# Optimization experiments

Measured on AMD Instinct MI355X. Metric: run time of the kernel, lower is better.

The kernel has to match this reference:

```python
import math
import jax, jax.numpy as jnp
import numpy as np

B, S, H, DQ, DV = 2, 2048, 16, 192, 128
NEG_INF = jnp.float32(-1e30)


def setup_inputs() -> dict:
    key = jax.random.key(0)
    kq, kk, kv = jax.random.split(key, 3)
    q = jax.random.normal(kq, (B, S, H, DQ), dtype=jnp.float32)
    k = jax.random.normal(kk, (B, S, H, DQ), dtype=jnp.float32)
    v = jax.random.normal(kv, (B, S, H, DV), dtype=jnp.float32)
    return {"q": q, "k": k, "v": v}


def reference(q, k, v):
    # Causal MLA attention, BSHD layout, asymmetric QK vs V head dims.
    dq = q.shape[-1]
    scale = jnp.asarray(math.sqrt(1.0 / dq), dtype=q.dtype)  # default 1/sqrt(dq)
    # scores: [B, H, S, S]
    scores = jnp.einsum("bqhd,bkhd->bhqk", q, k) * scale
    s = q.shape[1]
    causal = jnp.tril(jnp.ones((s, s), dtype=bool))  # qidx >= kidx
    scores = jnp.where(causal[None, None, :, :], scores, NEG_INF)
    p = jax.nn.softmax(scores, axis=-1)
    # out: [B, S, H, DV]
    out = jnp.einsum("bhqk,bkhd->bqhd", p, v)
    return out
```

## Files before the change

### kernel.cpp

```cpp
#include <hip/hip_runtime.h>

#define B_ 2
#define S_ 2048
#define H_ 16
#define DQ_ 192
#define DV_ 128
#define SCL2 0.10411163731422901f

typedef short short8 __attribute__((ext_vector_type(8)));
typedef float f32x4 __attribute__((ext_vector_type(4)));
typedef float f32x16 __attribute__((ext_vector_type(16)));
typedef unsigned uint2v __attribute__((ext_vector_type(2)));

#define KG_BYTES ((size_t)25165824)
#define VG_BYTES ((size_t)16777216)

__device__ __forceinline__ unsigned short f2bf(float f) {
  union { float f; unsigned u; } x; x.f = f;
  unsigned r = x.u + 0x7FFFu + ((x.u >> 16) & 1u);
  return (unsigned short)(r >> 16);
}

__device__ __forceinline__ float hw_exp2(float x) {
  float r; asm("v_exp_f32 %0, %1" : "=v"(r) : "v"(x)); return r;
}
__device__ __forceinline__ unsigned cvtpk(float lo, float hi) {
  unsigned r; asm("v_cvt_pk_bf16_f32 %0, %1, %2" : "=v"(r) : "v"(lo), "v"(hi)); return r;
}
__device__ __forceinline__ float pl32max(float x) {
  uint2v r = __builtin_amdgcn_permlane32_swap(__float_as_uint(x), __float_as_uint(x), false, false);
  return fmaxf(__uint_as_float(r[0]), __uint_as_float(r[1]));
}
__device__ __forceinline__ float pl32add(float x) {
  uint2v r = __builtin_amdgcn_permlane32_swap(__float_as_uint(x), __float_as_uint(x), false, false);
  return __uint_as_float(r[0]) + __uint_as_float(r[1]);
}

#define GLL16(src, dst) \
  __builtin_amdgcn_global_load_lds((const __attribute__((address_space(1))) void*)(src), \
                                   (__attribute__((address_space(3))) void*)(dst), 16, 0, 0)

__global__ __launch_bounds__(256) void prep_k(const float* __restrict__ K,
                                              unsigned short* __restrict__ Kg) {
  int idx = blockIdx.x * 256 + threadIdx.x;
  int d4 = idx % 48; int r = idx / 48;
  int h = r % H_; r /= H_;
  int s = r % S_; int b = r / S_;
  float4 f = *(const float4*)(K + (size_t)((b * S_ + s) * H_ + h) * DQ_ + d4 * 4);
  ushort4 u; u.x = f2bf(f.x); u.y = f2bf(f.y); u.z = f2bf(f.z); u.w = f2bf(f.w);
  size_t rowb = (size_t)((b * H_ + h) * S_ + s) * (DQ_ * 2);
  int cb = (d4 * 8) ^ ((s & 7) << 4);
  *(ushort4*)((char*)Kg + rowb + cb) = u;
}

__global__ __launch_bounds__(256) void prep_v(const float* __restrict__ V,
                                              unsigned short* __restrict__ Vg) {
  __shared__ float lv[64][132];
  int blk = blockIdx.x;
  int tile = blk & 31, bh = blk >> 5;
  int b = bh >> 4, h = bh & 15;
  int tid = threadIdx.x;
  #pragma unroll
  for (int it = 0; it < 8; ++it) {
    int idx = it * 256 + tid;
    int s_in = idx >> 5, d4 = idx & 31;
    float4 f = *(const float4*)(V + (size_t)((b * S_ + tile * 64 + s_in) * H_ + h) * DV_ + d4 * 4);
    lv[s_in][d4 * 4 + 0] = f.x; lv[s_in][d4 * 4 + 1] = f.y;
    lv[s_in][d4 * 4 + 2] = f.z; lv[s_in][d4 * 4 + 3] = f.w;
  }
  __syncthreads();
  char* base = (char*)Vg + (size_t)blk * 16384;
  #pragma unroll
  for (int it = 0; it < 4; ++it) {
    int ch = it * 256 + tid;
    int pr = ch >> 4, ci = ch & 15;
    int orig = ci ^ (pr & 15);
    int dv = pr * 2 + (orig >> 3);
    int k0 = (orig & 7) * 8;
    short8 u;
    #pragma unroll
    for (int e = 0; e < 8; ++e) u[e] = (short)f2bf(lv[k0 + e][dv]);
    *(short8*)(base + ch * 16) = u;
  }
}

__launch_bounds__(256, 2)
__global__ void mla_fwd(const float* __restrict__ Q,
                        const unsigned short* __restrict__ Kg,
                        const unsigned short* __restrict__ Vg,
                        float* __restrict__ O) {
  __shared__ __align__(16) unsigned char SB[2][40960];

  const int tid  = threadIdx.x;
  const int wid  = tid >> 6;
  const int lane = tid & 63;
  const int l31  = lane & 31;
  const int hi   = lane >> 5;
  const int hi16 = hi * 16;

  const int i  = blockIdx.x;
  const int x  = i & 7;
  const int li = i >> 3;
  const int r_ = li >> 5;
  const int c  = li & 31;
  const int bh = x * 4 + (c >> 3);
  const int jj = c & 7;
  const int qtile = r_ ? jj : (15 - jj);
  const int b  = bh >> 4, h = bh & 15;

  const char* kg_bh = (const char*)Kg + (size_t)bh * S_ * (DQ_ * 2);
  const char* vg_bh = (const char*)Vg + (size_t)bh * 32 * 16384;

  const int wq0 = qtile * 128 + wid * 32;
  const int qln = wq0 + l31;

  short8 qf[12];
  {
    const size_t qoff = (size_t)((b * S_ + qln) * H_ + h) * DQ_;
    #pragma unroll
    for (int d0 = 0; d0 < 12; ++d0) {
      const float* p = Q + qoff + d0 * 16 + hi * 8;
      float4 f0 = *(const float4*)(p);
      float4 f1 = *(const float4*)(p + 4);
      short8 a;
      a[0] = f2bf(f0.x * SCL2); a[1] = f2bf(f0.y * SCL2);
      a[2] = f2bf(f0.z * SCL2); a[3] = f2bf(f0.w * SCL2);
      a[4] = f2bf(f1.x * SCL2); a[5] = f2bf(f1.y * SCL2);
      a[6] = f2bf(f1.z * SCL2); a[7] = f2bf(f1.w * SCL2);
      qf[d0] = a;
    }
  }

  f32x16 o[4];
  #pragma unroll
  for (int t2 = 0; t2 < 4; ++t2) o[t2] = (f32x16)0.0f;
  float m = -1e30f, l = 0.0f;

  const int kxor = (lane & 7) << 4;
  const int prl  = l31 >> 1;
  const int nb_  = (lane & 1) * 8 + hi;
  int voff[2][2];
  #pragma unroll
  for (int kh = 0; kh < 2; ++kh)
    #pragma unroll
    for (int ks = 0; ks < 2; ++ks) {
      int n = nb_ + kh * 4 + ks * 2;
      voff[kh][ks] = prl * 256 + ((n ^ prl) << 4);
    }

  const int ntiles = 2 * qtile + 2;

  const char* kS = kg_bh + wid * 10240 + lane * 16;
  const char* vS = vg_bh - 24576 + wid * 10240 + lane * 16;

  #define STAGE(buf)                                                       \
    do {                                                                   \
      _Pragma("unroll")                                                    \
      for (int ci = 0; ci < 10; ++ci) {                                    \
        const int cc = wid * 10 + ci;                                      \
        const char* src = (cc < 24) ? (kS + ci * 1024) : (vS + ci * 1024); \
        GLL16(src, &SB[buf][cc * 1024]);                                   \
      }                                                                    \
    } while (0)

  #define HALF(S, KH)                                                             \
    {                                                                             \
      const int khb = kbase + (KH) * 32;                                          \
      if (khb <= wq0 + 31) {                                                      \
        float p_[16];                                                             \
        _Pragma("unroll") for (int r = 0; r < 16; ++r) p_[r] = S[r];              \
        if (khb + 31 > wq0) {                                                     \
          const int rem = qln - khb - 4 * hi;                                     \
          _Pragma("unroll") for (int r = 0; r < 16; ++r) {                        \
            const int kof = (r & 3) + 8 * (r >> 2);                               \
            if (kof > rem) p_[r] = -1e30f;                                        \
          }                                                                       \
        }                                                                         \
        float mx = p_[0];                                                         \
        _Pragma("unroll") for (int r = 1; r < 16; ++r) mx = fmaxf(mx, p_[r]);     \
        mx = pl32max(mx);                                                         \
        if (__any(mx > m + 8.0f)) {                                               \
          float mn = fmaxf(m, mx);                                                \
          float al = hw_exp2(m - mn);                                             \
          _Pragma("unroll") for (int t2 = 0; t2 < 4; ++t2) o[t2] *= al;           \
          l *= al; m = mn;                                                        \
        }                                                                         \
        _Pragma("unroll") for (int r = 0; r < 16; ++r) p_[r] = hw_exp2(p_[r] - m);\
        float sum_ = 0.0f;                                                        \
        _Pragma("unroll") for (int r = 0; r < 16; ++r) sum_ += p_[r];             \
        l += sum_;                                                                \
        unsigned a_ = cvtpk(p_[0], p_[1]),   b2_ = cvtpk(p_[2], p_[3]);           \
        unsigned c_ = cvtpk(p_[4], p_[5]),   d_  = cvtpk(p_[6], p_[7]);           \
        unsigned e_ = cvtpk(p_[8], p_[9]),   f_  = cvtpk(p_[10], p_[11]);         \
        unsigned g_ = cvtpk(p_[12], p_[13]), h_  = cvtpk(p_[14], p_[15]);         \
        uint2v s02 = __builtin_amdgcn_permlane32_swap(a_, c_, false, false);      \
        uint2v s13 = __builtin_amdgcn_permlane32_swap(b2_, d_, false, false);     \
        uint2v s46 = __builtin_amdgcn_permlane32_swap(e_, g_, false, false);      \
        uint2v s57 = __builtin_amdgcn_permlane32_swap(f_, h_, false, false);      \
        union { unsigned u[4]; short8 s; } pb0, pb1;                              \
        pb0.u[0] = s02[0]; pb0.u[1] = s13[0]; pb0.u[2] = s02[1]; pb0.u[3] = s13[1];\
        pb1.u[0] = s46[0]; pb1.u[1] = s57[0]; pb1.u[2] = s46[1]; pb1.u[3] = s57[1];\
        __builtin_amdgcn_s_setprio(1);                                            \
        _Pragma("unroll") for (int t2 = 0; t2 < 4; ++t2) {                        \
          short8 va0 = *(const short8*)(vbb + t2 * 4096 + voff[KH][0]);           \
          o[t2] = __builtin_amdgcn_mfma_f32_32x32x16_bf16(va0, pb0.s, o[t2], 0, 0, 0); \
          short8 va1 = *(const short8*)(vbb + t2 * 4096 + voff[KH][1]);           \
          o[t2] = __builtin_amdgcn_mfma_f32_32x32x16_bf16(va1, pb1.s, o[t2], 0, 0, 0); \
        }                                                                         \
        __builtin_amdgcn_s_setprio(0);                                            \
      }                                                                           \
    }

  STAGE(0); kS += 24576; vS += 16384;
  __syncthreads();

  int cur = 0;
  for (int kt = 0; kt < ntiles; ++kt) {
    const int kbase = kt * 64;
    if (kt + 1 < ntiles) { STAGE(cur ^ 1); kS += 24576; vS += 16384; }

    const unsigned char* kb  = SB[cur];
    const unsigned char* vbb = SB[cur] + 24576;
    const bool active = (kbase <= wq0 + 31);

    if (active) {
      const char* kr0 = (const char*)kb + l31 * 384;
      const char* kr1 = kr0 + 32 * 384;
      f32x16 s0 = (f32x16)0.0f, s1 = (f32x16)0.0f;
      __builtin_amdgcn_s_setprio(1);
      #pragma unroll
      for (int d0 = 0; d0 < 12; ++d0) {
        const int col = (d0 * 32 + hi16) ^ kxor;
        s0 = __builtin_amdgcn_mfma_f32_32x32x16_bf16(*(const short8*)(kr0 + col), qf[d0], s0, 0, 0, 0);
        s1 = __builtin_amdgcn_mfma_f32_32x32x16_bf16(*(const short8*)(kr1 + col), qf[d0], s1, 0, 0, 0);
      }
      __builtin_amdgcn_s_setprio(0);

      HALF(s0, 0)
      HALF(s1, 1)
    }

    __syncthreads();
    cur ^= 1;
  }

  {
    float ll = pl32add(l);
    const float inv = 1.0f / ll;
    float* ob = O + (size_t)((b * S_ + qln) * H_ + h) * DV_;
    #pragma unroll
    for (int t2 = 0; t2 < 4; ++t2) {
      #pragma unroll
      for (int rr = 0; rr < 4; ++rr) {
        float4 st = { o[t2][rr * 4 + 0] * inv, o[t2][rr * 4 + 1] * inv,
                      o[t2][rr * 4 + 2] * inv, o[t2][rr * 4 + 3] * inv };
        *(float4*)(ob + t2 * 32 + rr * 8 + hi * 4) = st;
      }
    }
  }
  #undef STAGE
  #undef HALF
}

__launch_bounds__(256)
__global__ void mla_fwd_fb(const float* __restrict__ Q,
                           const float* __restrict__ K,
                           const float* __restrict__ V,
                           float* __restrict__ O) {
  __shared__ __align__(16) unsigned short Kl[2][32][200];
  __shared__ __align__(16) unsigned short Vt[2][128][40];
  __shared__ __align__(16) unsigned short Pl[4][16][40];
  const int tid = threadIdx.x, wid = tid >> 6, lane = tid & 63;
  const int l15 = lane & 15, g = lane >> 4;
  const int qtile = (int)gridDim.x - 1 - (int)blockIdx.x;
  const int bh = blockIdx.y, b = bh >> 4, h = bh & 15;
  const int q0w = qtile * 64 + wid * 16;
  const int krs = H_ * DQ_, vrs = H_ * DV_;
  short8 aq[6];
  {
    const int qoff = ((b * S_ + (q0w + l15)) * H_ + h) * DQ_;
    #pragma unroll
    for (int d0 = 0; d0 < 6; ++d0) {
      const float* p = Q + qoff + d0 * 32 + g * 8;
      float4 f0 = *(const float4*)(p); float4 f1 = *(const float4*)(p + 4);
      short8 a;
      a[0]=f2bf(f0.x); a[1]=f2bf(f0.y); a[2]=f2bf(f0.z); a[3]=f2bf(f0.w);
      a[4]=f2bf(f1.x); a[5]=f2bf(f1.y); a[6]=f2bf(f1.z); a[7]=f2bf(f1.w);
      aq[d0] = a;
    }
  }
  f32x4 o[8];
  #pragma unroll
  for (int t = 0; t < 8; ++t) o[t] = (f32x4)0.0f;
  float m[4], l[4];
  #pragma unroll
  for (int r = 0; r < 4; ++r) { m[r] = -1e30f; l[r] = 0.0f; }
  const int ntiles = qtile * 2 + 2;
  float4 kr[6], vr[4];
  {
    const float* Kb = K + ((b * S_) * H_ + h) * DQ_;
    #pragma unroll
    for (int i = 0; i < 6; ++i) { int idx = i*256+tid; int row = idx/48, c4 = idx%48;
      kr[i] = *(const float4*)(Kb + row*krs + c4*4); }
    const float* Vb = V + ((b * S_) * H_ + h) * DV_;
    #pragma unroll
    for (int i = 0; i < 4; ++i) { int idx = i*256+tid; int row = idx&31, c4 = idx>>5;
      vr[i] = *(const float4*)(Vb + row*vrs + c4*4); }
    #pragma unroll
    for (int i = 0; i < 6; ++i) { int idx = i*256+tid; int row = idx/48, c4 = idx%48;
      ushort4 u; u.x=f2bf(kr[i].x); u.y=f2bf(kr[i].y); u.z=f2bf(kr[i].z); u.w=f2bf(kr[i].w);
      *(ushort4*)&Kl[0][row][c4*4] = u; }
    #pragma unroll
    for (int i = 0; i < 4; ++i) { int idx = i*256+tid; int row = idx&31, c4 = idx>>5;
      Vt[0][c4*4+0][row]=f2bf(vr[i].x); Vt[0][c4*4+1][row]=f2bf(vr[i].y);
      Vt[0][c4*4+2][row]=f2bf(vr[i].z); Vt[0][c4*4+3][row]=f2bf(vr[i].w); }
  }
  __syncthreads();
  int cur = 0;
  for (int kt = 0; kt < ntiles; ++kt) {
    const int kbase = kt * 32;
    const bool pf = (kt + 1 < ntiles);
    if (pf) {
      const int nb = kbase + 32;
      const float* Kb = K + ((b*S_+nb)*H_ + h)*DQ_;
      #pragma unroll
      for (int i = 0; i < 6; ++i) { int idx = i*256+tid; int row = idx/48, c4 = idx%48;
        kr[i] = *(const float4*)(Kb + row*krs + c4*4); }
      const float* Vb = V + ((b*S_+nb)*H_ + h)*DV_;
      #pragma unroll
      for (int i = 0; i < 4; ++i) { int idx = i*256+tid; int row = idx&31, c4 = idx>>5;
        vr[i] = *(const float4*)(Vb + row*vrs + c4*4); }
    }
    f32x4 sa0 = (f32x4)0.0f, sa1 = (f32x4)0.0f;
    #pragma unroll
    for (int d0 = 0; d0 < 6; ++d0) {
      short8 b0 = *(const short8*)&Kl[cur][l15][d0*32 + g*8];
      sa0 = __builtin_amdgcn_mfma_f32_16x16x32_bf16(aq[d0], b0, sa0, 0, 0, 0);
      short8 b1 = *(const short8*)&Kl[cur][16+l15][d0*32 + g*8];
      sa1 = __builtin_amdgcn_mfma_f32_16x16x32_bf16(aq[d0], b1, sa1, 0, 0, 0);
    }
    float p0[4], p1[4];
    #pragma unroll
    for (int r = 0; r < 4; ++r) {
      const int qg = q0w + 4*g + r;
      float s0 = sa0[r]*SCL2, s1 = sa1[r]*SCL2;
      if (kbase + l15 > qg) s0 = -1e30f;
      if (kbase + 16 + l15 > qg) s1 = -1e30f;
      p0[r] = s0; p1[r] = s1;
    }
    #pragma unroll
    for (int r = 0; r < 4; ++r) {
      float rm = fmaxf(p0[r], p1[r]);
      #pragma unroll
      for (int off = 1; off < 16; off <<= 1) rm = fmaxf(rm, __shfl_xor(rm, off));
      float mn = fmaxf(m[r], rm);
      float alpha = exp2f(m[r] - mn); m[r] = mn;
      float e0 = exp2f(p0[r] - mn), e1 = exp2f(p1[r] - mn);
      p0[r] = e0; p1[r] = e1;
      float rsum = e0 + e1;
      #pragma unroll
      for (int off = 1; off < 16; off <<= 1) rsum += __shfl_xor(rsum, off);
      l[r] = l[r]*alpha + rsum;
      #pragma unroll
      for (int t = 0; t < 8; ++t) o[t][r] *= alpha;
    }
    #pragma unroll
    for (int r = 0; r < 4; ++r) {
      Pl[wid][4*g+r][l15]      = f2bf(p0[r]);
      Pl[wid][4*g+r][16+l15]   = f2bf(p1[r]);
    }
    short8 pa = *(const short8*)&Pl[wid][l15][g*8];
    #pragma unroll
    for (int t = 0; t < 8; ++t) {
      short8 vb = *(const short8*)&Vt[cur][t*16+l15][g*8];
      o[t] = __builtin_amdgcn_mfma_f32_16x16x32_bf16(pa, vb, o[t], 0, 0, 0);
    }
    if (pf) {
      #pragma unroll
      for (int i = 0; i < 6; ++i) { int idx = i*256+tid; int row = idx/48, c4 = idx%48;
        ushort4 u; u.x=f2bf(kr[i].x); u.y=f2bf(kr[i].y); u.z=f2bf(kr[i].z); u.w=f2bf(kr[i].w);
        *(ushort4*)&Kl[cur^1][row][c4*4] = u; }
      #pragma unroll
      for (int i = 0; i < 4; ++i) { int idx = i*256+tid; int row = idx&31, c4 = idx>>5;
        Vt[cur^1][c4*4+0][row]=f2bf(vr[i].x); Vt[cur^1][c4*4+1][row]=f2bf(vr[i].y);
        Vt[cur^1][c4*4+2][row]=f2bf(vr[i].z); Vt[cur^1][c4*4+3][row]=f2bf(vr[i].w); }
    }
    __syncthreads();
    cur ^= 1;
  }
  #pragma unroll
  for (int r = 0; r < 4; ++r) {
    const int qg = q0w + 4*g + r;
    const float inv = 1.0f / l[r];
    #pragma unroll
    for (int t = 0; t < 8; ++t)
      O[((b*S_+qg)*H_ + h)*DV_ + t*16 + l15] = o[t][r] * inv;
  }
}

extern "C" void kernel_launch(void* const* d_in, const int* in_sizes, int n_in,
                              void* d_out, int out_size, void* d_ws, size_t ws_size,
                              hipStream_t stream) {
  const float* q = (const float*)d_in[0];
  const float* k = (const float*)d_in[1];
  const float* v = (const float*)d_in[2];
  float* out = (float*)d_out;

  if (ws_size >= KG_BYTES + VG_BYTES) {
    unsigned short* Kg = (unsigned short*)d_ws;
    unsigned short* Vg = (unsigned short*)((char*)d_ws + KG_BYTES);
    prep_k<<<dim3((B_ * S_ * H_ * 48) / 256), dim3(256), 0, stream>>>(k, Kg);
    prep_v<<<dim3(B_ * H_ * 32), dim3(256), 0, stream>>>(v, Vg);
    mla_fwd<<<dim3(512), dim3(256), 0, stream>>>(q, Kg, Vg, out);
  } else {
    dim3 grid(S_ / 64, B_ * H_);
    mla_fwd_fb<<<grid, dim3(256), 0, stream>>>(q, k, v, out);
  }
}
```

Measured before the change: 94.97 us.

## Read V fragments directly from global memory and merge softmax over 64-key tile

Stops staging V tiles into shared memory. Each wave now loads its V MFMA operands straight from the pre-swizzled global bf16 buffer, which cuts the LDS footprint from 40KB to 24KB per buffer. The two 32-key softmax halves are merged into one 64-key pass with a tree max and tree sum, so there is one rescale check per tile. The block-to-tile mapping is also changed so causal q-tiles are interleaved across heads differently. In exchange, V reads now depend on global/L2 latency inside the inner loop instead of being prefetched into LDS.

```diff
diff --git a/kernel.cpp b/kernel.cpp
--- a/kernel.cpp
+++ b/kernel.cpp
@@ -89,7 +89,7 @@
                         const unsigned short* __restrict__ Kg,
                         const unsigned short* __restrict__ Vg,
                         float* __restrict__ O) {
-  __shared__ __align__(16) unsigned char SB[2][40960];
+  __shared__ __align__(16) unsigned char SB[2][24576];
 
   const int tid  = threadIdx.x;
   const int wid  = tid >> 6;
@@ -103,15 +103,15 @@
   const int li = i >> 3;
   const int r_ = li >> 5;
   const int c  = li & 31;
-  const int bh = x * 4 + (c >> 3);
-  const int jj = c & 7;
-  const int qtile = r_ ? jj : (15 - jj);
+  const int qt = c & 15;
+  const int pid = c >> 4;
+  const int bh = x * 4 + pid * 2 + r_;
   const int b  = bh >> 4, h = bh & 15;
 
   const char* kg_bh = (const char*)Kg + (size_t)bh * S_ * (DQ_ * 2);
   const char* vg_bh = (const char*)Vg + (size_t)bh * 32 * 16384;
 
-  const int wq0 = qtile * 128 + wid * 32;
+  const int wq0 = qt * 128 + wid * 32;
   const int qln = wq0 + l31;
 
   short8 qf[12];
@@ -148,83 +148,31 @@
       voff[kh][ks] = prl * 256 + ((n ^ prl) << 4);
     }
 
-  const int ntiles = 2 * qtile + 2;
-
-  const char* kS = kg_bh + wid * 10240 + lane * 16;
-  const char* vS = vg_bh - 24576 + wid * 10240 + lane * 16;
-
-  #define STAGE(buf)                                                       \
-    do {                                                                   \
-      _Pragma("unroll")                                                    \
-      for (int ci = 0; ci < 10; ++ci) {                                    \
-        const int cc = wid * 10 + ci;                                      \
-        const char* src = (cc < 24) ? (kS + ci * 1024) : (vS + ci * 1024); \
-        GLL16(src, &SB[buf][cc * 1024]);                                   \
-      }                                                                    \
+  const int ntiles = 2 * qt + 2;
+
+  const char* kS = kg_bh + wid * 6144 + lane * 16;
+  const int sdo = wid * 6144;
+
+  #define STAGE(buf)                                        \
+    do {                                                    \
+      _Pragma("unroll")                                     \
+      for (int ci = 0; ci < 6; ++ci)                        \
+        GLL16(kS + ci * 1024, &SB[buf][sdo + ci * 1024]);   \
     } while (0)
 
-  #define HALF(S, KH)                                                             \
-    {                                                                             \
-      const int khb = kbase + (KH) * 32;                                          \
-      if (khb <= wq0 + 31) {                                                      \
-        float p_[16];                                                             \
-        _Pragma("unroll") for (int r = 0; r < 16; ++r) p_[r] = S[r];              \
-        if (khb + 31 > wq0) {                                                     \
-          const int rem = qln - khb - 4 * hi;                                     \
-          _Pragma("unroll") for (int r = 0; r < 16; ++r) {                        \
-            const int kof = (r & 3) + 8 * (r >> 2);                               \
-            if (kof > rem) p_[r] = -1e30f;                                        \
-          }                                                                       \
-        }                                                                         \
-        float mx = p_[0];                                                         \
-        _Pragma("unroll") for (int r = 1; r < 16; ++r) mx = fmaxf(mx, p_[r]);     \
-        mx = pl32max(mx);                                                         \
-        if (__any(mx > m + 8.0f)) {                                               \
-          float mn = fmaxf(m, mx);                                                \
-          float al = hw_exp2(m - mn);                                             \
-          _Pragma("unroll") for (int t2 = 0; t2 < 4; ++t2) o[t2] *= al;           \
-          l *= al; m = mn;                                                        \
-        }                                                                         \
-        _Pragma("unroll") for (int r = 0; r < 16; ++r) p_[r] = hw_exp2(p_[r] - m);\
-        float sum_ = 0.0f;                                                        \
-        _Pragma("unroll") for (int r = 0; r < 16; ++r) sum_ += p_[r];             \
-        l += sum_;                                                                \
-        unsigned a_ = cvtpk(p_[0], p_[1]),   b2_ = cvtpk(p_[2], p_[3]);           \
-        unsigned c_ = cvtpk(p_[4], p_[5]),   d_  = cvtpk(p_[6], p_[7]);           \
-        unsigned e_ = cvtpk(p_[8], p_[9]),   f_  = cvtpk(p_[10], p_[11]);         \
-        unsigned g_ = cvtpk(p_[12], p_[13]), h_  = cvtpk(p_[14], p_[15]);         \
-        uint2v s02 = __builtin_amdgcn_permlane32_swap(a_, c_, false, false);      \
-        uint2v s13 = __builtin_amdgcn_permlane32_swap(b2_, d_, false, false);     \
-        uint2v s46 = __builtin_amdgcn_permlane32_swap(e_, g_, false, false);      \
-        uint2v s57 = __builtin_amdgcn_permlane32_swap(f_, h_, false, false);      \
-        union { unsigned u[4]; short8 s; } pb0, pb1;                              \
-        pb0.u[0] = s02[0]; pb0.u[1] = s13[0]; pb0.u[2] = s02[1]; pb0.u[3] = s13[1];\
-        pb1.u[0] = s46[0]; pb1.u[1] = s57[0]; pb1.u[2] = s46[1]; pb1.u[3] = s57[1];\
-        __builtin_amdgcn_s_setprio(1);                                            \
-        _Pragma("unroll") for (int t2 = 0; t2 < 4; ++t2) {                        \
-          short8 va0 = *(const short8*)(vbb + t2 * 4096 + voff[KH][0]);           \
-          o[t2] = __builtin_amdgcn_mfma_f32_32x32x16_bf16(va0, pb0.s, o[t2], 0, 0, 0); \
-          short8 va1 = *(const short8*)(vbb + t2 * 4096 + voff[KH][1]);           \
-          o[t2] = __builtin_amdgcn_mfma_f32_32x32x16_bf16(va1, pb1.s, o[t2], 0, 0, 0); \
-        }                                                                         \
-        __builtin_amdgcn_s_setprio(0);                                            \
-      }                                                                           \
-    }
-
-  STAGE(0); kS += 24576; vS += 16384;
+  STAGE(0); kS += 24576;
   __syncthreads();
 
   int cur = 0;
   for (int kt = 0; kt < ntiles; ++kt) {
     const int kbase = kt * 64;
-    if (kt + 1 < ntiles) { STAGE(cur ^ 1); kS += 24576; vS += 16384; }
-
-    const unsigned char* kb  = SB[cur];
-    const unsigned char* vbb = SB[cur] + 24576;
+    if (kt + 1 < ntiles) { STAGE(cur ^ 1); kS += 24576; }
+
+    const char* vgt = (const char*)vg_bh + (size_t)kt * 16384;
     const bool active = (kbase <= wq0 + 31);
 
     if (active) {
-      const char* kr0 = (const char*)kb + l31 * 384;
+      const char* kr0 = (const char*)&SB[cur][0] + l31 * 384;
       const char* kr1 = kr0 + 32 * 384;
       f32x16 s0 = (f32x16)0.0f, s1 = (f32x16)0.0f;
       __builtin_amdgcn_s_setprio(1);
@@ -236,8 +184,112 @@
       }
       __builtin_amdgcn_s_setprio(0);
 
-      HALF(s0, 0)
-      HALF(s1, 1)
+      short8 v00 = *(const short8*)(vgt + 0 * 4096 + voff[0][0]);
+      short8 v01 = *(const short8*)(vgt + 0 * 4096 + voff[0][1]);
+      short8 v10 = *(const short8*)(vgt + 1 * 4096 + voff[0][0]);
+      short8 v11 = *(const short8*)(vgt + 1 * 4096 + voff[0][1]);
+      short8 v20 = *(const short8*)(vgt + 2 * 4096 + voff[0][0]);
+      short8 v21 = *(const short8*)(vgt + 2 * 4096 + voff[0][1]);
+      short8 v30 = *(const short8*)(vgt + 3 * 4096 + voff[0][0]);
+      short8 v31 = *(const short8*)(vgt + 3 * 4096 + voff[0][1]);
+
+      float p_[32];
+      #pragma unroll
+      for (int r = 0; r < 16; ++r) { p_[r] = s0[r]; p_[16 + r] = s1[r]; }
+      if (kbase + 63 > wq0) {
+        const int rem = qln - kbase - 4 * hi;
+        #pragma unroll
+        for (int r = 0; r < 16; ++r) {
+          const int kof = (r & 3) + 8 * (r >> 2);
+          if (kof > rem)      p_[r]      = -1e30f;
+          if (kof + 32 > rem) p_[16 + r] = -1e30f;
+        }
+      }
+
+      float t16[16];
+      #pragma unroll
+      for (int r = 0; r < 16; ++r) t16[r] = fmaxf(p_[r], p_[16 + r]);
+      float t8[8];
+      #pragma unroll
+      for (int r = 0; r < 8; ++r) t8[r] = fmaxf(t16[r], t16[8 + r]);
+      float t4[4];
+      #pragma unroll
+      for (int r = 0; r < 4; ++r) t4[r] = fmaxf(t8[r], t8[4 + r]);
+      float mx = fmaxf(fmaxf(t4[0], t4[1]), fmaxf(t4[2], t4[3]));
+      mx = pl32max(mx);
+      if (__any(mx > m + 8.0f)) {
+        float mn = fmaxf(m, mx);
+        float al = hw_exp2(m - mn);
+        #pragma unroll
+        for (int t2 = 0; t2 < 4; ++t2) o[t2] *= al;
+        l *= al; m = mn;
+      }
+      #pragma unroll
+      for (int jj = 0; jj < 32; ++jj) p_[jj] = hw_exp2(p_[jj] - m);
+      float a16[16];
+      #pragma unroll
+      for (int r = 0; r < 16; ++r) a16[r] = p_[r] + p_[16 + r];
+      float a8[8];
+      #pragma unroll
+      for (int r = 0; r < 8; ++r) a8[r] = a16[r] + a16[8 + r];
+      float a4[4];
+      #pragma unroll
+      for (int r = 0; r < 4; ++r) a4[r] = a8[r] + a8[4 + r];
+      l += (a4[0] + a4[1]) + (a4[2] + a4[3]);
+
+      short8 w00 = *(const short8*)(vgt + 0 * 4096 + voff[1][0]);
+      short8 w01 = *(const short8*)(vgt + 0 * 4096 + voff[1][1]);
+      short8 w10 = *(const short8*)(vgt + 1 * 4096 + voff[1][0]);
+      short8 w11 = *(const short8*)(vgt + 1 * 4096 + voff[1][1]);
+      short8 w20 = *(const short8*)(vgt + 2 * 4096 + voff[1][0]);
+      short8 w21 = *(const short8*)(vgt + 2 * 4096 + voff[1][1]);
+      short8 w30 = *(const short8*)(vgt + 3 * 4096 + voff[1][0]);
+      short8 w31 = *(const short8*)(vgt + 3 * 4096 + voff[1][1]);
+
+      union { unsigned u[4]; short8 s; } pb00, pb01, pb10, pb11;
+      {
+        unsigned a_ = cvtpk(p_[0], p_[1]),   b2_ = cvtpk(p_[2], p_[3]);
+        unsigned c_ = cvtpk(p_[4], p_[5]),   d_  = cvtpk(p_[6], p_[7]);
+        unsigned e_ = cvtpk(p_[8], p_[9]),   f_  = cvtpk(p_[10], p_[11]);
+        unsigned g_ = cvtpk(p_[12], p_[13]), h_  = cvtpk(p_[14], p_[15]);
+        uint2v s02 = __builtin_amdgcn_permlane32_swap(a_, c_, false, false);
+        uint2v s13 = __builtin_amdgcn_permlane32_swap(b2_, d_, false, false);
+        uint2v s46 = __builtin_amdgcn_permlane32_swap(e_, g_, false, false);
+        uint2v s57 = __builtin_amdgcn_permlane32_swap(f_, h_, false, false);
+        pb00.u[0] = s02[0]; pb00.u[1] = s13[0]; pb00.u[2] = s02[1]; pb00.u[3] = s13[1];
+        pb01.u[0] = s46[0]; pb01.u[1] = s57[0]; pb01.u[2] = s46[1]; pb01.u[3] = s57[1];
+      }
+      {
+        unsigned a_ = cvtpk(p_[16], p_[17]), b2_ = cvtpk(p_[18], p_[19]);
+        unsigned c_ = cvtpk(p_[20], p_[21]), d_  = cvtpk(p_[22], p_[23]);
+        unsigned e_ = cvtpk(p_[24], p_[25]), f_  = cvtpk(p_[26], p_[27]);
+        unsigned g_ = cvtpk(p_[28], p_[29]), h_  = cvtpk(p_[30], p_[31]);
+        uint2v s02 = __builtin_amdgcn_permlane32_swap(a_, c_, false, false);
+        uint2v s13 = __builtin_amdgcn_permlane32_swap(b2_, d_, false, false);
+        uint2v s46 = __builtin_amdgcn_permlane32_swap(e_, g_, false, false);
+        uint2v s57 = __builtin_amdgcn_permlane32_swap(f_, h_, false, false);
+        pb10.u[0] = s02[0]; pb10.u[1] = s13[0]; pb10.u[2] = s02[1]; pb10.u[3] = s13[1];
+        pb11.u[0] = s46[0]; pb11.u[1] = s57[0]; pb11.u[2] = s46[1]; pb11.u[3] = s57[1];
+      }
+
+      __builtin_amdgcn_s_setprio(1);
+      o[0] = __builtin_amdgcn_mfma_f32_32x32x16_bf16(v00, pb00.s, o[0], 0, 0, 0);
+      o[0] = __builtin_amdgcn_mfma_f32_32x32x16_bf16(v01, pb01.s, o[0], 0, 0, 0);
+      o[1] = __builtin_amdgcn_mfma_f32_32x32x16_bf16(v10, pb00.s, o[1], 0, 0, 0);
+      o[1] = __builtin_amdgcn_mfma_f32_32x32x16_bf16(v11, pb01.s, o[1], 0, 0, 0);
+      o[2] = __builtin_amdgcn_mfma_f32_32x32x16_bf16(v20, pb00.s, o[2], 0, 0, 0);
+      o[2] = __builtin_amdgcn_mfma_f32_32x32x16_bf16(v21, pb01.s, o[2], 0, 0, 0);
+      o[3] = __builtin_amdgcn_mfma_f32_32x32x16_bf16(v30, pb00.s, o[3], 0, 0, 0);
+      o[3] = __builtin_amdgcn_mfma_f32_32x32x16_bf16(v31, pb01.s, o[3], 0, 0, 0);
+      o[0] = __builtin_amdgcn_mfma_f32_32x32x16_bf16(w00, pb10.s, o[0], 0, 0, 0);
+      o[0] = __builtin_amdgcn_mfma_f32_32x32x16_bf16(w01, pb11.s, o[0], 0, 0, 0);
+      o[1] = __builtin_amdgcn_mfma_f32_32x32x16_bf16(w10, pb10.s, o[1], 0, 0, 0);
+      o[1] = __builtin_amdgcn_mfma_f32_32x32x16_bf16(w11, pb11.s, o[1], 0, 0, 0);
+      o[2] = __builtin_amdgcn_mfma_f32_32x32x16_bf16(w20, pb10.s, o[2], 0, 0, 0);
+      o[2] = __builtin_amdgcn_mfma_f32_32x32x16_bf16(w21, pb11.s, o[2], 0, 0, 0);
+      o[3] = __builtin_amdgcn_mfma_f32_32x32x16_bf16(w30, pb10.s, o[3], 0, 0, 0);
+      o[3] = __builtin_amdgcn_mfma_f32_32x32x16_bf16(w31, pb11.s, o[3], 0, 0, 0);
+      __builtin_amdgcn_s_setprio(0);
     }
 
     __syncthreads();
@@ -259,7 +311,6 @@
     }
   }
   #undef STAGE
-  #undef HALF
 }
 
 __launch_bounds__(256)
```

Result: slower. 132.4 us (+39.4%).
